# Performance work log

Measured on AMD Instinct MI355X. Metric: run time of the kernel, lower is better.

## Reference

```python
import jax, jax.numpy as jnp
import numpy as np

NUM_GROUPS = 32
EPS = 1e-6
NUM_HEADS = 8


def group_norm32(x, gamma, beta):
    # GroupNorm32: compute in float32, cast back to input dtype.
    b, c, h, w = x.shape
    xf = x.astype(jnp.float32).reshape(b, NUM_GROUPS, -1)  # [b, G, (C/G)*h*w]
    mean = xf.mean(axis=-1, keepdims=True)
    var = xf.var(axis=-1, keepdims=True)
    xn = ((xf - mean) * jax.lax.rsqrt(var + EPS)).reshape(b, c, h, w)
    xn = xn * gamma[None, :, None, None] + beta[None, :, None, None]
    return xn.astype(x.dtype)


def setup_inputs() -> dict:
    key = jax.random.key(0)
    ks = jax.random.split(key, 4)
    b, c, h, w = 16, 512, 32, 32
    x = jax.random.normal(ks[0], (b, c, h, w), dtype=jnp.float32)
    w_qkv = jax.random.normal(ks[1], (3 * c, c), dtype=jnp.float32) * (1.0 / np.sqrt(c))
    b_qkv = jnp.zeros((3 * c,), dtype=jnp.float32)
    w_proj = jax.random.normal(ks[2], (c, c), dtype=jnp.float32) * (1.0 / np.sqrt(c))
    b_proj = jnp.zeros((c,), dtype=jnp.float32)
    gamma = jnp.ones((c,), dtype=jnp.float32)
    beta = jnp.zeros((c,), dtype=jnp.float32)
    return {"x": x, "w_qkv": w_qkv, "b_qkv": b_qkv, "w_proj": w_proj,
            "b_proj": b_proj, "gamma": gamma, "beta": beta}


def reference(x, w_qkv, b_qkv, w_proj, b_proj, gamma, beta):
    b, c, h, w = x.shape
    H = NUM_HEADS
    d = c // H
    n = h * w
    x_norm = group_norm32(x, gamma, beta)
    # 1x1 conv == channel matmul
    qkv = jnp.einsum('oc,bchw->bohw', w_qkv, x_norm) + b_qkv[None, :, None, None]
    q, k, v = jnp.split(qkv, 3, axis=1)
    q = q.reshape(b, H, d, n)
    k = k.reshape(b, H, d, n)
    v = v.reshape(b, H, d, n)
    scale = d ** (-0.5)
    attn = jnp.einsum('bhdn,bhdm->bhnm', q, k) * scale  # [b,H,n,n]
    attn = jax.nn.softmax(attn, axis=-1)
    out = jnp.einsum('bhnm,bhdm->bhdn', attn, v).reshape(b, c, h, w)
    proj = jnp.einsum('oc,bchw->bohw', w_proj, out) + b_proj[None, :, None, None]
    return x + proj
```

## Files before the change

kernel.cpp:

```cpp
#include <hip/hip_runtime.h>
#include <hip/hip_bf16.h>

typedef __bf16 bf16;
typedef __bf16 bf16x4 __attribute__((ext_vector_type(4)));
typedef __bf16 bf16x8 __attribute__((ext_vector_type(8)));
typedef float  floatx4 __attribute__((ext_vector_type(4)));
typedef float  f32x16  __attribute__((ext_vector_type(16)));

#define BB   16
#define CC   512
#define NN   1024
#define GG   32
#define CPG  16
#define HH   8
#define DD   64
#define QSCALE 0.18033688011f

#if __has_builtin(__builtin_amdgcn_exp2f)
#define EXP2(x) __builtin_amdgcn_exp2f(x)
#else
#define EXP2(x) exp2f(x)
#endif

__device__ inline floatx4 mfma16(bf16x8 a, bf16x8 b, floatx4 c) {
    return __builtin_amdgcn_mfma_f32_16x16x32_bf16(a, b, c, 0, 0, 0);
}
__device__ inline f32x16 mfma32(bf16x8 a, bf16x8 b, f32x16 c) {
    return __builtin_amdgcn_mfma_f32_32x32x16_bf16(a, b, c, 0, 0, 0);
}

__device__ inline floatx4 zero4() {
    floatx4 z; z[0] = 0.f; z[1] = 0.f; z[2] = 0.f; z[3] = 0.f; return z;
}

__device__ inline void gl_lds16(const bf16* g, bf16* l) {
    __builtin_amdgcn_global_load_lds(
        (const __attribute__((address_space(1))) unsigned int*)g,
        (__attribute__((address_space(3))) unsigned int*)l, 16, 0, 0);
}

__device__ inline unsigned cvt_pk_bf16(float a, float b) {
    unsigned r;
    asm("v_cvt_pk_bf16_f32 %0, %1, %2" : "=v"(r) : "v"(a), "v"(b));
    return r;
}
__device__ inline void pl32swap(unsigned &x, unsigned &y) {
    asm volatile("v_permlane32_swap_b32 %0, %1" : "+v"(x), "+v"(y));
}

__device__ inline float ldf(const void* p, size_t i, int isb) {
    return isb ? (float)((const bf16*)p)[i] : ((const float*)p)[i];
}
__device__ inline floatx4 ldf4(const void* p, size_t i, int isb) {
    floatx4 o;
    if (isb) {
        bf16x4 v = *(const bf16x4*)((const bf16*)p + i);
        #pragma unroll
        for (int j = 0; j < 4; ++j) o[j] = (float)v[j];
    } else {
        o = *(const floatx4*)((const float*)p + i);
    }
    return o;
}
__device__ inline void stf(void* p, size_t i, float v, int isb) {
    if (isb) ((bf16*)p)[i] = (bf16)v; else ((float*)p)[i] = v;
}

__global__ __launch_bounds__(256) void flag_kernel(const void* x, const void* wq,
        const void* wp, const void* gamma, int* flags) {
    __shared__ int bad[3];
    const int tid = threadIdx.x;
    if (tid < 3) bad[tid] = 0;
    __syncthreads();
    const void* arrs[3] = {x, wq, wp};
    #pragma unroll
    for (int a = 0; a < 3; ++a) {
        const unsigned short* u = (const unsigned short*)arrs[a];
        int c = 0;
        for (int i = tid * 32; i < tid * 32 + 32; ++i) {
            if ((u[i] & 0x7F80) == 0x7F80) c = 1;
        }
        if (c) atomicOr(&bad[a], 1);
    }
    __syncthreads();
    if (tid == 0) {
        flags[0] = bad[0] ? 0 : 1;
        flags[1] = bad[1] ? 0 : 1;
        flags[2] = bad[2] ? 0 : 1;
        flags[3] = (((const unsigned short*)gamma)[0] == 0x3F80) ? 1 : 0;
    }
}

__global__ __launch_bounds__(256) void cvt_kernel(const void* __restrict__ src,
        bf16* __restrict__ dst, int n, const int* __restrict__ flags, int fidx) {
    const int f = flags[fidx];
    int i = (blockIdx.x * 256 + threadIdx.x) * 4;
    if (i >= n) return;
    if (f) {
        *(bf16x4*)(dst + i) = *(const bf16x4*)((const bf16*)src + i);
    } else {
        const float* s = (const float*)src + i;
        bf16x4 o;
        #pragma unroll
        for (int j = 0; j < 4; ++j) o[j] = (bf16)s[j];
        *(bf16x4*)(dst + i) = o;
    }
}

__global__ __launch_bounds__(256) void gn_kernel(const void* __restrict__ x,
        const void* __restrict__ gamma, const void* __restrict__ beta,
        bf16* __restrict__ xn_t, const int* __restrict__ flags, int b0) {
    const int fx = flags[0], fg = flags[3];
    const int bg = blockIdx.x;
    const int bl = bg >> 5, g = bg & 31;
    const int tid = threadIdx.x;
    const size_t xbase = (size_t)((b0 + bl) * CC + g * CPG) * NN;

    float s = 0.f, ss = 0.f;
    for (int i = tid * 4; i < CPG * NN; i += 1024) {
        floatx4 v = ldf4(x, xbase + i, fx);
        #pragma unroll
        for (int j = 0; j < 4; ++j) { s += v[j]; ss += v[j] * v[j]; }
    }
    for (int off = 32; off > 0; off >>= 1) {
        s  += __shfl_down(s, off);
        ss += __shfl_down(ss, off);
    }
    __shared__ float red[8];
    __shared__ float stats[2];
    const int wave = tid >> 6;
    if ((tid & 63) == 0) { red[wave] = s; red[4 + wave] = ss; }
    __syncthreads();
    if (tid == 0) {
        float S  = red[0] + red[1] + red[2] + red[3];
        float SS = red[4] + red[5] + red[6] + red[7];
        float mean = S * (1.0f / (CPG * NN));
        float var  = SS * (1.0f / (CPG * NN)) - mean * mean;
        stats[0] = mean;
        stats[1] = rsqrtf(fmaxf(var, 0.f) + 1e-6f);
    }
    __syncthreads();
    const float mean = stats[0], rstd = stats[1];

    __shared__ __align__(16) float tile[CPG][64];
    const int cn = tid >> 4;
    const int nb = (tid & 15) * 4;
    const float gm1 = ldf(gamma, g * CPG + cn, fg);
    const float bt1 = ldf(beta,  g * CPG + cn, fg);
    const int n2 = tid >> 2, cq = tid & 3;
    for (int nt = 0; nt < NN / 64; ++nt) {
        floatx4 v = ldf4(x, xbase + (size_t)cn * NN + nt * 64 + nb, fx);
        #pragma unroll
        for (int j = 0; j < 4; ++j)
            tile[cn][nb + j] = (v[j] - mean) * rstd * gm1 + bt1;
        __syncthreads();
        bf16x4 o;
        #pragma unroll
        for (int k = 0; k < 4; ++k) o[k] = (bf16)tile[cq * 4 + k][n2];
        *(bf16x4*)(xn_t + (size_t)(bl * NN + nt * 64 + n2) * CC + g * CPG + cq * 4) = o;
        __syncthreads();
    }
}

__global__ __launch_bounds__(256) void qkv_kernel(const bf16* __restrict__ wq_b,
        const bf16* __restrict__ b_qkv, const bf16* __restrict__ xn_t,
        bf16* __restrict__ q_t, bf16* __restrict__ k_t, bf16* __restrict__ v_m) {
    __shared__ __align__(16) bf16 As[128 * 32];
    __shared__ __align__(16) bf16 Bs[128 * 32];

    const int ntile = blockIdx.x;
    const int mtile = blockIdx.y;
    const int bl = blockIdx.z;
    const int w = threadIdx.x >> 6, lane = threadIdx.x & 63;
    const int l16 = lane & 15, quad = lane >> 4;
    const int wr = w >> 1, wc = w & 1;

    const int mbase = mtile * 128, nbase = ntile * 128;
    const int srow = lane >> 2, scol = (lane & 3) * 8;
    const bf16* Ag = wq_b + (size_t)(mbase + w * 32 + srow) * CC + scol;
    const bf16* Bg = xn_t + (size_t)bl * NN * CC + (size_t)(nbase + w * 32 + srow) * CC + scol;
    bf16* Al = As + (2 * w) * 512;
    bf16* Bl = Bs + (2 * w) * 512;

    floatx4 acc[4][4];
    #pragma unroll
    for (int i = 0; i < 4; ++i)
        #pragma unroll
        for (int j = 0; j < 4; ++j) acc[i][j] = zero4();

    for (int k0 = 0; k0 < CC; k0 += 32) {
        __syncthreads();
        gl_lds16(Ag + k0, Al);
        gl_lds16(Ag + 16 * CC + k0, Al + 512);
        gl_lds16(Bg + k0, Bl);
        gl_lds16(Bg + 16 * CC + k0, Bl + 512);
        __syncthreads();

        bf16x8 af[4], bfr[4];
        #pragma unroll
        for (int mt = 0; mt < 4; ++mt)
            af[mt] = *(const bf16x8*)&As[(wr * 64 + mt * 16 + l16) * 32 + quad * 8];
        #pragma unroll
        for (int nt = 0; nt < 4; ++nt)
            bfr[nt] = *(const bf16x8*)&Bs[(wc * 64 + nt * 16 + l16) * 32 + quad * 8];
        #pragma unroll
        for (int mt = 0; mt < 4; ++mt)
            #pragma unroll
            for (int nt = 0; nt < 4; ++nt)
                acc[mt][nt] = mfma16(af[mt], bfr[nt], acc[mt][nt]);
    }

    const int qsel = mtile >> 2;
    const int obase = (mtile & 3) * 128;
    #pragma unroll
    for (int mt = 0; mt < 4; ++mt) {
        const int op = obase + wr * 64 + mt * 16 + quad * 4;
        float bias[4];
        #pragma unroll
        for (int r = 0; r < 4; ++r) bias[r] = (float)b_qkv[qsel * CC + op + r];
        #pragma unroll
        for (int nt = 0; nt < 4; ++nt) {
            const int p = nbase + wc * 64 + nt * 16 + l16;
            if (qsel == 0) {
                int h = op >> 6, d0 = op & 63;
                bf16x4 o;
                #pragma unroll
                for (int r = 0; r < 4; ++r) o[r] = (bf16)((acc[mt][nt][r] + bias[r]) * QSCALE);
                *(bf16x4*)(q_t + ((size_t)(bl * HH + h) * NN + p) * DD + d0) = o;
            } else if (qsel == 1) {
                int h = op >> 6, d0 = op & 63;
                bf16x4 o;
                #pragma unroll
                for (int r = 0; r < 4; ++r) o[r] = (bf16)(acc[mt][nt][r] + bias[r]);
                *(bf16x4*)(k_t + ((size_t)(bl * HH + h) * NN + p) * DD + d0) = o;
            } else {
                #pragma unroll
                for (int r = 0; r < 4; ++r)
                    v_m[((size_t)bl * CC + op + r) * NN + p] = (bf16)(acc[mt][nt][r] + bias[r]);
            }
        }
    }
}

__global__ __launch_bounds__(256) void attn_kernel(const bf16* __restrict__ q_t,
        const bf16* __restrict__ k_t, const bf16* __restrict__ v_m,
        bf16* __restrict__ attn_out) {
    const int qb = blockIdx.x;
    const int bh = blockIdx.y;
    const int bl = bh >> 3, h = bh & 7;
    const int tid = threadIdx.x;
    const int w = tid >> 6, lane = tid & 63;
    const int l31 = lane & 31, hi = lane >> 5;

    __shared__ __align__(16) bf16 Kt[2][64 * 64];
    __shared__ __align__(16) bf16 Vt[2][64 * 64];

    const bf16* kb = k_t + (size_t)bh * NN * DD;
    const bf16* vb = v_m + (size_t)bh * DD * NN;

    const int r8 = lane >> 3, sl = lane & 7;
    const int gcol = ((sl ^ r8) << 3);
    const int w16 = w * 16;

#define STAGE(buf, m0) do {                                                       \
    gl_lds16(kb + (size_t)((m0) + w16 + r8) * DD + gcol,     &Kt[buf][(w16) * 64]);     \
    gl_lds16(kb + (size_t)((m0) + w16 + 8 + r8) * DD + gcol, &Kt[buf][(w16 + 8) * 64]); \
    gl_lds16(vb + (size_t)(w16 + r8) * NN + (m0) + gcol,     &Vt[buf][(w16) * 64]);     \
    gl_lds16(vb + (size_t)(w16 + 8 + r8) * NN + (m0) + gcol, &Vt[buf][(w16 + 8) * 64]); \
} while (0)

    const int qrow = qb * 128 + w * 32 + l31;
    const bf16* qp = q_t + ((size_t)bh * NN + qrow) * DD + hi * 8;
    bf16x8 qf[4];
    #pragma unroll
    for (int ks = 0; ks < 4; ++ks) qf[ks] = *(const bf16x8*)(qp + ks * 16);

    f32x16 oacc[2];
    #pragma unroll
    for (int i = 0; i < 2; ++i)
        #pragma unroll
        for (int r = 0; r < 16; ++r) oacc[i][r] = 0.f;
    float lrun = 0.f;

    STAGE(0, 0);

    for (int it = 0; it < 16; ++it) {
        const int cur = it & 1;
        const int nm0 = ((it + 1) & 15) * 64;
        STAGE(cur ^ 1, nm0);
        asm volatile("s_waitcnt vmcnt(4)" ::: "memory");
        __builtin_amdgcn_s_barrier();
        asm volatile("" ::: "memory");

        const bf16* KtB = Kt[cur];
        const bf16* VtB = Vt[cur];

        #pragma unroll
        for (int kb2 = 0; kb2 < 2; ++kb2) {
            const int krow = kb2 * 32 + l31;
            const int ksw = krow & 7;
            f32x16 s;
            #pragma unroll
            for (int r = 0; r < 16; ++r) s[r] = 0.f;
            #pragma unroll
            for (int ks = 0; ks < 4; ++ks) {
                bf16x8 kf = *(const bf16x8*)(KtB + krow * 64 + (((2 * ks + hi) ^ ksw) << 3));
                s = mfma32(kf, qf[ks], s);
            }
            float p[16];
            #pragma unroll
            for (int r = 0; r < 16; ++r) { p[r] = EXP2(s[r]); lrun += p[r]; }
            unsigned pw[8];
            #pragma unroll
            for (int i = 0; i < 8; ++i) pw[i] = cvt_pk_bf16(p[2 * i], p[2 * i + 1]);
            pl32swap(pw[0], pw[2]); pl32swap(pw[1], pw[3]);
            pl32swap(pw[4], pw[6]); pl32swap(pw[5], pw[7]);

            #pragma unroll
            for (int tt = 0; tt < 2; ++tt) {
                union { unsigned u[4]; bf16x8 v; } pf;
                pf.u[0] = pw[tt * 4 + 0]; pf.u[1] = pw[tt * 4 + 1];
                pf.u[2] = pw[tt * 4 + 2]; pf.u[3] = pw[tt * 4 + 3];
                const int t = kb2 * 2 + tt;
                #pragma unroll
                for (int db = 0; db < 2; ++db) {
                    const int vrow = db * 32 + l31;
                    bf16x8 vf = *(const bf16x8*)(VtB + vrow * 64 +
                                                 (((2 * t + hi) ^ (vrow & 7)) << 3));
                    oacc[db] = mfma32(vf, pf.v, oacc[db]);
                }
            }
        }
        asm volatile("s_waitcnt lgkmcnt(0)" ::: "memory");
        __builtin_amdgcn_s_barrier();
        asm volatile("" ::: "memory");
    }
#undef STAGE

    lrun += __shfl_xor(lrun, 32);
    const float inv = 1.0f / lrun;
    bf16* ob = attn_out + ((size_t)bl * NN + qrow) * CC + h * DD;
    #pragma unroll
    for (int db = 0; db < 2; ++db) {
        #pragma unroll
        for (int g = 0; g < 4; ++g) {
            bf16x4 o;
            #pragma unroll
            for (int e = 0; e < 4; ++e) o[e] = (bf16)(oacc[db][4 * g + e] * inv);
            *(bf16x4*)(ob + db * 32 + g * 8 + hi * 4) = o;
        }
    }
}

__global__ __launch_bounds__(256) void proj_kernel(const bf16* __restrict__ wp_b,
        const bf16* __restrict__ b_proj, const bf16* __restrict__ attn_out,
        const void* __restrict__ x, void* __restrict__ out,
        const int* __restrict__ flags, int b0) {
    __shared__ __align__(16) bf16 As[128 * 32];
    __shared__ __align__(16) bf16 Bs[128 * 32];

    const int fx = flags[0];
    const int ntile = blockIdx.x;
    const int mtile = blockIdx.y;
    const int bl = blockIdx.z;
    const int w = threadIdx.x >> 6, lane = threadIdx.x & 63;
    const int l16 = lane & 15, quad = lane >> 4;
    const int wr = w >> 1, wc = w & 1;

    const int mbase = mtile * 128, nbase = ntile * 128;
    const int srow = lane >> 2, scol = (lane & 3) * 8;
    const bf16* Ag = wp_b + (size_t)(mbase + w * 32 + srow) * CC + scol;
    const bf16* Bg = attn_out + (size_t)bl * NN * CC + (size_t)(nbase + w * 32 + srow) * CC + scol;
    bf16* Al = As + (2 * w) * 512;
    bf16* Bl = Bs + (2 * w) * 512;

    floatx4 acc[4][4];
    #pragma unroll
    for (int i = 0; i < 4; ++i)
        #pragma unroll
        for (int j = 0; j < 4; ++j) acc[i][j] = zero4();

    for (int k0 = 0; k0 < CC; k0 += 32) {
        __syncthreads();
        gl_lds16(Ag + k0, Al);
        gl_lds16(Ag + 16 * CC + k0, Al + 512);
        gl_lds16(Bg + k0, Bl);
        gl_lds16(Bg + 16 * CC + k0, Bl + 512);
        __syncthreads();

        bf16x8 af[4], bfr[4];
        #pragma unroll
        for (int mt = 0; mt < 4; ++mt)
            af[mt] = *(const bf16x8*)&As[(wr * 64 + mt * 16 + l16) * 32 + quad * 8];
        #pragma unroll
        for (int nt = 0; nt < 4; ++nt)
            bfr[nt] = *(const bf16x8*)&Bs[(wc * 64 + nt * 16 + l16) * 32 + quad * 8];
        #pragma unroll
        for (int mt = 0; mt < 4; ++mt)
            #pragma unroll
            for (int nt = 0; nt < 4; ++nt)
                acc[mt][nt] = mfma16(af[mt], bfr[nt], acc[mt][nt]);
    }

    #pragma unroll
    for (int mt = 0; mt < 4; ++mt) {
        const int op = mbase + wr * 64 + mt * 16 + quad * 4;
        float bias[4];
        #pragma unroll
        for (int r = 0; r < 4; ++r) bias[r] = (float)b_proj[op + r];
        #pragma unroll
        for (int nt = 0; nt < 4; ++nt) {
            const int p = nbase + wc * 64 + nt * 16 + l16;
            #pragma unroll
            for (int r = 0; r < 4; ++r) {
                size_t idx = ((size_t)(b0 + bl) * CC + op + r) * NN + p;
                float xv = ldf(x, idx, fx);
                stf(out, idx, xv + acc[mt][nt][r] + bias[r], fx);
            }
        }
    }
}

extern "C" void kernel_launch(void* const* d_in, const int* in_sizes, int n_in,
                              void* d_out, int out_size, void* d_ws, size_t ws_size,
                              hipStream_t stream) {
    const void* x      = d_in[0];
    const void* w_qkv  = d_in[1];
    const bf16* b_qkv  = (const bf16*)d_in[2];
    const void* w_proj = d_in[3];
    const bf16* b_proj = (const bf16*)d_in[4];
    const void* gamma  = d_in[5];
    const void* beta   = d_in[6];

    const size_t MB = (size_t)1 << 20;
    const int NQKV = 3 * CC * CC;
    const int NPRJ = CC * CC;
    const size_t wbytes = (size_t)(NQKV + NPRJ) * sizeof(bf16) + 4096;
    int bc = 0;
    for (int c = 16; c >= 1; c >>= 1) {
        if ((size_t)c * 4 * MB + wbytes <= ws_size) { bc = c; break; }
    }
    if (bc == 0) {
        hipMemsetAsync(d_out, 0, (size_t)out_size * sizeof(bf16), stream);
        return;
    }

    const size_t cs = (size_t)bc * MB;
    char* ws = (char*)d_ws;
    bf16* xn_t = (bf16*)(ws);
    bf16* q_t  = (bf16*)(ws + cs);
    bf16* k_t  = (bf16*)(ws + 2 * cs);
    bf16* v_m  = (bf16*)(ws + 3 * cs);
    int*  flags = (int*)(ws + 4 * cs);
    bf16* wq_b = (bf16*)(ws + 4 * cs + 4096);
    bf16* wp_b = wq_b + NQKV;
    bf16* attn_out = xn_t;

    flag_kernel<<<1, 256, 0, stream>>>(x, w_qkv, w_proj, gamma, flags);
    cvt_kernel<<<NQKV / 1024, 256, 0, stream>>>(w_qkv, wq_b, NQKV, flags, 1);
    cvt_kernel<<<NPRJ / 1024, 256, 0, stream>>>(w_proj, wp_b, NPRJ, flags, 2);

    for (int b0 = 0; b0 < BB; b0 += bc) {
        gn_kernel<<<dim3(bc * GG), 256, 0, stream>>>(x, gamma, beta, xn_t, flags, b0);
        qkv_kernel<<<dim3(8, 12, bc), 256, 0, stream>>>(wq_b, b_qkv, xn_t, q_t, k_t, v_m);
        attn_kernel<<<dim3(8, bc * HH), 256, 0, stream>>>(q_t, k_t, v_m, attn_out);
        proj_kernel<<<dim3(8, 4, bc), 256, 0, stream>>>(wp_b, b_proj, attn_out, x, d_out, flags, b0);
    }
}
```

Measured before the change: 245.8 us.

## Double-buffer LDS loads and XOR-swizzle tiles in QKV and projection GEMMs

The QKV and output-projection GEMM kernels now keep two LDS buffers, issuing the global-to-LDS copies for the next K slice before computing on the current one. Explicit vmcnt/lgkmcnt waits and raw barriers replace the two __syncthreads per iteration. The LDS column layout is XOR-swizzled on both store and load to reduce bank conflicts on the fragment reads. This doubles LDS use per block and adds one redundant prefetch on the final iteration, and correctness depends on the hand-set vmcnt counts matching the four outstanding loads.

After: 242.5 us. About the same (-1.4%).

```diff
diff --git a/kernel.cpp b/kernel.cpp
--- a/kernel.cpp
+++ b/kernel.cpp
@@ -165,8 +165,8 @@
 __global__ __launch_bounds__(256) void qkv_kernel(const bf16* __restrict__ wq_b,
         const bf16* __restrict__ b_qkv, const bf16* __restrict__ xn_t,
         bf16* __restrict__ q_t, bf16* __restrict__ k_t, bf16* __restrict__ v_m) {
-    __shared__ __align__(16) bf16 As[128 * 32];
-    __shared__ __align__(16) bf16 Bs[128 * 32];
+    __shared__ __align__(16) bf16 As[2][128 * 32];
+    __shared__ __align__(16) bf16 Bs[2][128 * 32];
 
     const int ntile = blockIdx.x;
     const int mtile = blockIdx.y;
@@ -176,11 +176,18 @@
     const int wr = w >> 1, wc = w & 1;
 
     const int mbase = mtile * 128, nbase = ntile * 128;
-    const int srow = lane >> 2, scol = (lane & 3) * 8;
+    const int srow = lane >> 2;
+    const int scol = (((lane & 3) ^ ((srow >> 1) & 3)) << 3);
     const bf16* Ag = wq_b + (size_t)(mbase + w * 32 + srow) * CC + scol;
     const bf16* Bg = xn_t + (size_t)bl * NN * CC + (size_t)(nbase + w * 32 + srow) * CC + scol;
-    bf16* Al = As + (2 * w) * 512;
-    bf16* Bl = Bs + (2 * w) * 512;
+    const int ldso = (2 * w) * 512;
+
+#define QSTAGE(buf, k0) do {                                  \
+    gl_lds16(Ag + (k0),           &As[buf][ldso]);            \
+    gl_lds16(Ag + 16 * CC + (k0), &As[buf][ldso + 512]);      \
+    gl_lds16(Bg + (k0),           &Bs[buf][ldso]);            \
+    gl_lds16(Bg + 16 * CC + (k0), &Bs[buf][ldso + 512]);      \
+} while (0)
 
     floatx4 acc[4][4];
     #pragma unroll
@@ -188,27 +195,34 @@
         #pragma unroll
         for (int j = 0; j < 4; ++j) acc[i][j] = zero4();
 
-    for (int k0 = 0; k0 < CC; k0 += 32) {
-        __syncthreads();
-        gl_lds16(Ag + k0, Al);
-        gl_lds16(Ag + 16 * CC + k0, Al + 512);
-        gl_lds16(Bg + k0, Bl);
-        gl_lds16(Bg + 16 * CC + k0, Bl + 512);
-        __syncthreads();
+    const int sw = (l16 >> 1) & 3;
+    QSTAGE(0, 0);
+
+    for (int it = 0; it < 16; ++it) {
+        const int cur = it & 1;
+        const int nk = ((it + 1) & 15) * 32;
+        QSTAGE(cur ^ 1, nk);
+        asm volatile("s_waitcnt vmcnt(4)" ::: "memory");
+        __builtin_amdgcn_s_barrier();
 
         bf16x8 af[4], bfr[4];
         #pragma unroll
         for (int mt = 0; mt < 4; ++mt)
-            af[mt] = *(const bf16x8*)&As[(wr * 64 + mt * 16 + l16) * 32 + quad * 8];
+            af[mt] = *(const bf16x8*)&As[cur][(wr * 64 + mt * 16 + l16) * 32 + ((quad ^ sw) << 3)];
         #pragma unroll
         for (int nt = 0; nt < 4; ++nt)
-            bfr[nt] = *(const bf16x8*)&Bs[(wc * 64 + nt * 16 + l16) * 32 + quad * 8];
+            bfr[nt] = *(const bf16x8*)&Bs[cur][(wc * 64 + nt * 16 + l16) * 32 + ((quad ^ sw) << 3)];
+
+        asm volatile("s_waitcnt lgkmcnt(0)" ::: "memory");
+        __builtin_amdgcn_s_barrier();
+
         #pragma unroll
         for (int mt = 0; mt < 4; ++mt)
             #pragma unroll
             for (int nt = 0; nt < 4; ++nt)
                 acc[mt][nt] = mfma16(af[mt], bfr[nt], acc[mt][nt]);
     }
+#undef QSTAGE
 
     const int qsel = mtile >> 2;
     const int obase = (mtile & 3) * 128;
@@ -356,8 +370,8 @@
         const bf16* __restrict__ b_proj, const bf16* __restrict__ attn_out,
         const void* __restrict__ x, void* __restrict__ out,
         const int* __restrict__ flags, int b0) {
-    __shared__ __align__(16) bf16 As[128 * 32];
-    __shared__ __align__(16) bf16 Bs[128 * 32];
+    __shared__ __align__(16) bf16 As[2][128 * 32];
+    __shared__ __align__(16) bf16 Bs[2][128 * 32];
 
     const int fx = flags[0];
     const int ntile = blockIdx.x;
@@ -368,11 +382,18 @@
     const int wr = w >> 1, wc = w & 1;
 
     const int mbase = mtile * 128, nbase = ntile * 128;
-    const int srow = lane >> 2, scol = (lane & 3) * 8;
+    const int srow = lane >> 2;
+    const int scol = (((lane & 3) ^ ((srow >> 1) & 3)) << 3);
     const bf16* Ag = wp_b + (size_t)(mbase + w * 32 + srow) * CC + scol;
     const bf16* Bg = attn_out + (size_t)bl * NN * CC + (size_t)(nbase + w * 32 + srow) * CC + scol;
-    bf16* Al = As + (2 * w) * 512;
-    bf16* Bl = Bs + (2 * w) * 512;
+    const int ldso = (2 * w) * 512;
+
+#define PSTAGE(buf, k0) do {                                  \
+    gl_lds16(Ag + (k0),           &As[buf][ldso]);            \
+    gl_lds16(Ag + 16 * CC + (k0), &As[buf][ldso + 512]);      \
+    gl_lds16(Bg + (k0),           &Bs[buf][ldso]);            \
+    gl_lds16(Bg + 16 * CC + (k0), &Bs[buf][ldso + 512]);      \
+} while (0)
 
     floatx4 acc[4][4];
     #pragma unroll
@@ -380,27 +401,34 @@
         #pragma unroll
         for (int j = 0; j < 4; ++j) acc[i][j] = zero4();
 
-    for (int k0 = 0; k0 < CC; k0 += 32) {
-        __syncthreads();
-        gl_lds16(Ag + k0, Al);
-        gl_lds16(Ag + 16 * CC + k0, Al + 512);
-        gl_lds16(Bg + k0, Bl);
-        gl_lds16(Bg + 16 * CC + k0, Bl + 512);
-        __syncthreads();
+    const int sw = (l16 >> 1) & 3;
+    PSTAGE(0, 0);
+
+    for (int it = 0; it < 16; ++it) {
+        const int cur = it & 1;
+        const int nk = ((it + 1) & 15) * 32;
+        PSTAGE(cur ^ 1, nk);
+        asm volatile("s_waitcnt vmcnt(4)" ::: "memory");
+        __builtin_amdgcn_s_barrier();
 
         bf16x8 af[4], bfr[4];
         #pragma unroll
         for (int mt = 0; mt < 4; ++mt)
-            af[mt] = *(const bf16x8*)&As[(wr * 64 + mt * 16 + l16) * 32 + quad * 8];
+            af[mt] = *(const bf16x8*)&As[cur][(wr * 64 + mt * 16 + l16) * 32 + ((quad ^ sw) << 3)];
         #pragma unroll
         for (int nt = 0; nt < 4; ++nt)
-            bfr[nt] = *(const bf16x8*)&Bs[(wc * 64 + nt * 16 + l16) * 32 + quad * 8];
+            bfr[nt] = *(const bf16x8*)&Bs[cur][(wc * 64 + nt * 16 + l16) * 32 + ((quad ^ sw) << 3)];
+
+        asm volatile("s_waitcnt lgkmcnt(0)" ::: "memory");
+        __builtin_amdgcn_s_barrier();
+
         #pragma unroll
         for (int mt = 0; mt < 4; ++mt)
             #pragma unroll
             for (int nt = 0; nt < 4; ++nt)
                 acc[mt][nt] = mfma16(af[mt], bfr[nt], acc[mt][nt]);
     }
+#undef PSTAGE
 
     #pragma unroll
     for (int mt = 0; mt < 4; ++mt) {
```
